# Optimization experiments

Measured on AMD Instinct MI355X. Metric: run time of the kernel, lower is better.

The kernel has to match this reference:

```python
import jax, jax.numpy as jnp
import numpy as np

EPS_NORM = 1e-12  # F.normalize eps
LN_EPS = 1e-5


def _ln(x, g, b):
    mu = x.mean(-1, keepdims=True)
    var = ((x - mu) ** 2).mean(-1, keepdims=True)
    return (x - mu) / jnp.sqrt(var + LN_EPS) * g + b


def _gate(x, w1, b1, g, b, w2, b2):
    # Linear -> LayerNorm(32) -> SiLU -> Linear -> Sigmoid, squeeze(-1)
    t = _ln(x @ w1 + b1, g, b)
    t = jax.nn.silu(t)
    return jax.nn.sigmoid(t @ w2 + b2)[..., 0]


def setup_inputs() -> dict:
    key = jax.random.key(0)
    B, N, D, dH, S, HID = 4, 4096, 1024, 256, 256, 32
    ks = jax.random.split(key, 24)
    sc_d = 0.5 * (6.0 / (D + dH)) ** 0.5  # xavier gain=0.5 approx
    sc_h = 0.5 * (6.0 / (D + HID)) ** 0.5
    inp = {
        "h": jax.random.normal(ks[0], (B, N, D), jnp.float32),
        # encoder complex projection (stored as (in,out))
        "Wr": jax.random.uniform(ks[1], (D, dH), jnp.float32, -sc_d, sc_d),
        "br": jnp.zeros((dH,), jnp.float32),
        "Wi": jax.random.uniform(ks[2], (D, dH), jnp.float32, -sc_d, sc_d),
        "bi": jnp.zeros((dH,), jnp.float32),
        # uncertainty net
        "uw1": jax.random.uniform(ks[3], (D, HID), jnp.float32, -sc_h, sc_h),
        "ub1": jnp.zeros((HID,), jnp.float32),
        "ug": jnp.ones((HID,), jnp.float32),
        "ubeta": jnp.zeros((HID,), jnp.float32),
        "uw2": jax.random.uniform(ks[4], (HID, 1), jnp.float32, -0.2, 0.2),
        "ub2": jnp.zeros((1,), jnp.float32),
        # decoherence gamma net
        "gw1": jax.random.uniform(ks[5], (D, HID), jnp.float32, -sc_h, sc_h),
        "gb1": jnp.zeros((HID,), jnp.float32),
        "gg": jnp.ones((HID,), jnp.float32),
        "gbeta": jnp.zeros((HID,), jnp.float32),
        "gw2": jax.random.uniform(ks[6], (HID, 1), jnp.float32, -0.2, 0.2),
        "gb2": jnp.zeros((1,), jnp.float32),
        # memory attention params
        "m_real": jax.random.normal(ks[7], (S, dH), jnp.float32) / dH ** 0.5,
        "m_imag": jax.random.normal(ks[8], (S, dH), jnp.float32) / dH ** 0.5,
        "values": jax.random.normal(ks[9], (S, D), jnp.float32) * 0.02,
        "ow": jax.random.uniform(ks[10], (D, D), jnp.float32, -0.5 * (3.0 / D) ** 0.5, 0.5 * (3.0 / D) ** 0.5),
        "ob": jnp.zeros((D,), jnp.float32),
        # norms
        "n1g": jnp.ones((D,), jnp.float32),
        "n1b": jnp.zeros((D,), jnp.float32),
        "n2g": jnp.ones((D,), jnp.float32),
        "n2b": jnp.zeros((D,), jnp.float32),
        # FFN
        "fw1": jax.random.normal(ks[11], (D, 4 * D), jnp.float32) * (2.0 / (5 * D)) ** 0.5,
        "fb1": jnp.zeros((4 * D,), jnp.float32),
        "fw2": jax.random.normal(ks[12], (4 * D, D), jnp.float32) * (2.0 / (5 * D)) ** 0.5,
        "fb2": jnp.zeros((D,), jnp.float32),
    }
    return inp


def reference(h, Wr, br, Wi, bi,
              uw1, ub1, ug, ubeta, uw2, ub2,
              gw1, gb1, gg, gbeta, gw2, gb2,
              m_real, m_imag, values, ow, ob,
              n1g, n1b, n2g, n2b, fw1, fb1, fw2, fb2):
    dH = m_real.shape[-1]
    # --- QuantumStateEncoder: psi = normalize(complex(Wr h, Wi h)), p in [0,0.95]
    pr = h @ Wr + br                       # (B,N,dH) real part
    pi = h @ Wi + bi                       # (B,N,dH) imag part
    nrm = jnp.maximum(jnp.sqrt(jnp.sum(pr * pr + pi * pi, -1, keepdims=True)), EPS_NORM)
    pr, pi = pr / nrm, pi / nrm
    p_init = _gate(h, uw1, ub1, ug, ubeta, uw2, ub2) * 0.95   # (B,N)
    # --- ContextualDecoherenceLayer: ctx = mean over N (identical per token)
    ctx = h.mean(axis=1)                   # (B,D)
    gamma = _gate(ctx, gw1, gb1, gg, gbeta, gw2, gb2)          # (B,)
    p = p_init * (1.0 - gamma[:, None])    # (B,N)
    # --- ExternalQuantumMemoryAttention
    mnrm = jnp.maximum(jnp.sqrt(jnp.sum(m_real * m_real + m_imag * m_imag, -1, keepdims=True)), EPS_NORM)
    Mr, Mi = m_real / mnrm, m_imag / mnrm  # (S,dH)
    # <psi|m> = sum conj(psi)*m ; |.|^2 is re^2+im^2
    re = jnp.einsum('bnd,sd->bns', pr, Mr) + jnp.einsum('bnd,sd->bns', pi, Mi)
    im = jnp.einsum('bnd,sd->bns', pr, Mi) - jnp.einsum('bnd,sd->bns', pi, Mr)
    overlap = re * re + im * im            # (B,N,S)
    raw = (1.0 - p)[..., None] * overlap + (p / dH)[..., None]
    attn = raw / (raw.sum(-1, keepdims=True) + 1e-8)
    attn_out = jnp.einsum('bns,sd->bnd', attn, values) @ ow + ob
    # --- residual + LN + FFN (dropout = eval identity)
    h1 = _ln(h + attn_out, n1g, n1b)
    ff = jax.nn.gelu(h1 @ fw1 + fb1, approximate=False) @ fw2 + fb2
    return _ln(h1 + ff, n2g, n2b)
```

## Files before the change

### kernel.cpp

```cpp
#include <hip/hip_runtime.h>
#include <math.h>


#define B_ 4
#define N_ 4096
#define D_ 1024
#define DH_ 256
#define S_ 256
#define HID_ 32
#define M_ (B_ * N_)

typedef unsigned short u16;
typedef unsigned int u32;
typedef __attribute__((ext_vector_type(8))) short bfrag;
typedef __attribute__((ext_vector_type(4))) float ffrag;

__device__ __forceinline__ float b2f(u16 u) {
    return __uint_as_float(((unsigned)u) << 16);
}
__device__ __forceinline__ u16 f2b(float f) {
    unsigned u = __float_as_uint(f);
    return (u16)((u + 0x7FFFu + ((u >> 16) & 1u)) >> 16);
}
__device__ __forceinline__ float fast_erf(float x) {
    float ax = fabsf(x);
    float t = __builtin_amdgcn_rcpf(fmaf(0.3275911f, ax, 1.f));
    float p = t * fmaf(t, fmaf(t, fmaf(t, fmaf(t, 1.061405429f, -1.453152027f),
                                       1.421413741f), -0.284496736f),
                       0.254829592f);
    float e = __expf(-ax * ax);
    float y = fmaf(-p, e, 1.f);
    return copysignf(y, x);
}
__device__ __forceinline__ float gelu_fast(float x) {
    return 0.5f * x * (1.0f + fast_erf(x * 0.70710678118654752440f));
}
__device__ __forceinline__ float ldf(const void* p, size_t i, bool bf) {
    return bf ? b2f(((const u16*)p)[i]) : ((const float*)p)[i];
}
__device__ __forceinline__ bool detect_bf(const void* n1g) {
    return *(const unsigned*)n1g == 0x3F803F80u;
}
__device__ __forceinline__ void gload16(const void* g, void* lds) {
    __builtin_amdgcn_global_load_lds(
        (const __attribute__((address_space(1))) u32*)g,
        (__attribute__((address_space(3))) u32*)lds, 16, 0, 0);
}

__global__ void zero_kernel(float* __restrict__ p, int n) {
    int i = blockIdx.x * 256 + threadIdx.x;
    if (i < n) p[i] = 0.f;
}

__global__ __launch_bounds__(256)
void h2b_kernel(const void* __restrict__ h, u16* __restrict__ hB,
                const void* __restrict__ n1g) {
    const bool bf = detect_bf(n1g);
    const size_t i = ((size_t)blockIdx.x * 256 + threadIdx.x) * 8;
    if (bf) {
        *(uint4*)(hB + i) = *(const uint4*)((const u16*)h + i);
    } else {
        const float* hf = (const float*)h;
        float4 x = *(const float4*)(hf + i);
        float4 y = *(const float4*)(hf + i + 4);
        union { u16 u[8]; uint4 v; } pk;
        pk.u[0] = f2b(x.x); pk.u[1] = f2b(x.y);
        pk.u[2] = f2b(x.z); pk.u[3] = f2b(x.w);
        pk.u[4] = f2b(y.x); pk.u[5] = f2b(y.y);
        pk.u[6] = f2b(y.z); pk.u[7] = f2b(y.w);
        *(uint4*)(hB + i) = pk.v;
    }
}

__global__ void pack_bias_kernel(const void* __restrict__ br,
                                 const void* __restrict__ bi,
                                 void* __restrict__ brbi,
                                 const void* __restrict__ n1g) {
    const bool bf = detect_bf(n1g);
    const int t = threadIdx.x;
    if (bf) {
        ((u16*)brbi)[t]       = ((const u16*)br)[t];
        ((u16*)brbi)[256 + t] = ((const u16*)bi)[t];
    } else {
        ((float*)brbi)[t]       = ((const float*)br)[t];
        ((float*)brbi)[256 + t] = ((const float*)bi)[t];
    }
}

__global__ __launch_bounds__(256)
void transpose_w_kernel(const void* __restrict__ W, u16* __restrict__ WT,
                        int K, int N, const void* __restrict__ n1g) {
    const bool bf = detect_bf(n1g);
    __shared__ u16 t[64][65];
    const int n0 = blockIdx.x * 64, k0 = blockIdx.y * 64;
    const int a = threadIdx.x & 63, b = threadIdx.x >> 6;
#pragma unroll
    for (int r = 0; r < 16; ++r) {
        int k = b * 16 + r;
        t[k][a] = f2b(ldf(W, (size_t)(k0 + k) * N + n0 + a, bf));
    }
    __syncthreads();
#pragma unroll
    for (int r = 0; r < 16; ++r) {
        int n = b * 16 + r;
        WT[(size_t)(n0 + n) * K + k0 + a] = t[a][n];
    }
}

__global__ __launch_bounds__(256)
void ctx_sum_kernel(const u16* __restrict__ hB, float* __restrict__ ctx) {
    const int chunks = N_ / 128;
    const int b = blockIdx.x / chunks;
    const int ch = blockIdx.x % chunks;
    const int tid = threadIdx.x;
    const size_t base = ((size_t)b * N_ + (size_t)ch * 128) * D_;
    float a[4] = {0.f, 0.f, 0.f, 0.f};
    for (int r = 0; r < 128; ++r)
#pragma unroll
        for (int q = 0; q < 4; ++q)
            a[q] += b2f(hB[base + (size_t)r * D_ + q * 256 + tid]);
#pragma unroll
    for (int q = 0; q < 4; ++q)
        atomicAdd(&ctx[b * D_ + q * 256 + tid], a[q]);
}

__global__ __launch_bounds__(128)
void gamma_gate_kernel(const float* __restrict__ ctx,
                       const void* __restrict__ w1, const void* __restrict__ b1,
                       const void* __restrict__ g, const void* __restrict__ beta,
                       const void* __restrict__ w2, const void* __restrict__ b2,
                       float* __restrict__ out, const void* __restrict__ n1g) {
    const bool bf = detect_bf(n1g);
    const int row = blockIdx.x;
    const int tid = threadIdx.x;
    const int col = tid & 31;
    const int chunk = tid >> 5;
    const float xscale = 1.f / (float)N_;

    float acc = 0.f;
    for (int k = chunk * 256; k < chunk * 256 + 256; ++k)
        acc += ctx[(size_t)row * D_ + k] * xscale * ldf(w1, (size_t)k * HID_ + col, bf);

    __shared__ float part[4][HID_];
    __shared__ float s[HID_];
    __shared__ float mu_s, rstd_s;
    part[chunk][col] = acc;
    __syncthreads();
    if (tid < HID_)
        s[tid] = part[0][tid] + part[1][tid] + part[2][tid] + part[3][tid]
               + ldf(b1, tid, bf);
    __syncthreads();
    if (tid == 0) {
        float m = 0.f;
        for (int i = 0; i < HID_; ++i) m += s[i];
        m /= (float)HID_;
        float var = 0.f;
        for (int i = 0; i < HID_; ++i) { float dd = s[i] - m; var += dd * dd; }
        var /= (float)HID_;
        mu_s = m;
        rstd_s = rsqrtf(var + 1e-5f);
    }
    __syncthreads();
    if (tid < HID_) {
        float v = (s[tid] - mu_s) * rstd_s * ldf(g, tid, bf) + ldf(beta, tid, bf);
        v = v / (1.f + expf(-v));
        s[tid] = v * ldf(w2, tid, bf);
    }
    __syncthreads();
    if (tid == 0) {
        float z = 0.f;
        for (int i = 0; i < HID_; ++i) z += s[i];
        z += ldf(b2, 0, bf);
        out[row] = 1.f / (1.f + expf(-z));
    }
}

__global__ __launch_bounds__(128)
void p_gate_kernel(const u16* __restrict__ hB,
                   const void* __restrict__ w1, const void* __restrict__ b1,
                   const void* __restrict__ g, const void* __restrict__ beta,
                   const void* __restrict__ w2, const void* __restrict__ b2,
                   float* __restrict__ out, const void* __restrict__ n1g) {
    const bool bf = detect_bf(n1g);
    const int row = blockIdx.x;
    const int tid = threadIdx.x;
    const int col = tid & 31;
    const int chunk = tid >> 5;

    float acc = 0.f;
    for (int k = chunk * 256; k < chunk * 256 + 256; ++k)
        acc += b2f(hB[(size_t)row * D_ + k]) * ldf(w1, (size_t)k * HID_ + col, bf);

    __shared__ float part[4][HID_];
    __shared__ float s[HID_];
    __shared__ float mu_s, rstd_s;
    part[chunk][col] = acc;
    __syncthreads();
    if (tid < HID_)
        s[tid] = part[0][tid] + part[1][tid] + part[2][tid] + part[3][tid]
               + ldf(b1, tid, bf);
    __syncthreads();
    if (tid == 0) {
        float m = 0.f;
        for (int i = 0; i < HID_; ++i) m += s[i];
        m /= (float)HID_;
        float var = 0.f;
        for (int i = 0; i < HID_; ++i) { float dd = s[i] - m; var += dd * dd; }
        var /= (float)HID_;
        mu_s = m;
        rstd_s = rsqrtf(var + 1e-5f);
    }
    __syncthreads();
    if (tid < HID_) {
        float v = (s[tid] - mu_s) * rstd_s * ldf(g, tid, bf) + ldf(beta, tid, bf);
        v = v / (1.f + expf(-v));
        s[tid] = v * ldf(w2, tid, bf);
    }
    __syncthreads();
    if (tid == 0) {
        float z = 0.f;
        for (int i = 0; i < HID_; ++i) z += s[i];
        z += ldf(b2, 0, bf);
        out[row] = 0.95f / (1.f + expf(-z));
    }
}

__global__ __launch_bounds__(256)
void norm_m_kernel(const void* __restrict__ m_real, const void* __restrict__ m_imag,
                   u16* __restrict__ bcatT, const void* __restrict__ n1g) {
    const bool bf = detect_bf(n1g);
    const int s = blockIdx.x;
    const int d = threadIdx.x;
    float mr = ldf(m_real, (size_t)s * DH_ + d, bf);
    float mi = ldf(m_imag, (size_t)s * DH_ + d, bf);
    float v = mr * mr + mi * mi;
#pragma unroll
    for (int off = 32; off; off >>= 1) v += __shfl_down(v, off, 64);
    __shared__ float red[4];
    if ((d & 63) == 0) red[d >> 6] = v;
    __syncthreads();
    float tot = red[0] + red[1] + red[2] + red[3];
    float inv = 1.f / fmaxf(sqrtf(tot), 1e-12f);
    float nr = mr * inv, ni = mi * inv;
    bcatT[(size_t)s * 512 + d]               = f2b(nr);
    bcatT[(size_t)s * 512 + 256 + d]         = f2b(ni);
    bcatT[(size_t)(256 + s) * 512 + d]       = f2b(ni);
    bcatT[(size_t)(256 + s) * 512 + 256 + d] = f2b(-nr);
}

__global__ __launch_bounds__(256)
void gemm_mfma(const u16* __restrict__ A, const u16* __restrict__ WT,
               const void* __restrict__ bias, void* __restrict__ out,
               int kseg, int lda, int ldw, int ldo,
               int act, int fo32, const void* __restrict__ n1g) {
    const bool bf = detect_bf(n1g);
    __shared__ short As[128 * 64];
    __shared__ short Bs[128 * 64];
    const int tid = threadIdx.x;

    const int nwg = gridDim.x * gridDim.y;
    const int flat = blockIdx.y * gridDim.x + blockIdx.x;
    const int xcd = flat & 7, idx = flat >> 3;
    const int qq = nwg >> 3, rr = nwg & 7;
    const int nf = (xcd < rr ? xcd * (qq + 1) : rr * (qq + 1) + (xcd - rr) * qq) + idx;
    const int c0 = (nf % gridDim.x) * 128;
    const int r0 = (nf / gridDim.x) * 128;

    const int lane = tid & 63, wave = tid >> 6;
    const int wm = wave & 1, wn = wave >> 1;
    const int quad = lane >> 4, l15 = lane & 15;
    const int l8 = lane >> 3;
    const int lc = (lane & 7) ^ l8;
    const int sx = l15 & 7;

    ffrag acc[4][4];
#pragma unroll
    for (int i = 0; i < 4; ++i)
#pragma unroll
        for (int j = 0; j < 4; ++j)
            acc[i][j] = (ffrag){0.f, 0.f, 0.f, 0.f};

    for (int k0 = 0; k0 < kseg; k0 += 64) {
        __syncthreads();
#pragma unroll
        for (int i = 0; i < 4; ++i) {
            int rb = wave * 32 + i * 8;
            gload16(A + (size_t)(r0 + rb + l8) * lda + k0 + lc * 8, &As[rb * 64]);
        }
#pragma unroll
        for (int i = 0; i < 4; ++i) {
            int rb = wave * 32 + i * 8;
            gload16(WT + (size_t)(c0 + rb + l8) * ldw + k0 + lc * 8, &Bs[rb * 64]);
        }
        __syncthreads();

#pragma unroll
        for (int ks = 0; ks < 2; ++ks) {
            bfrag a[4], b[4];
#pragma unroll
            for (int i = 0; i < 4; ++i) {
                int row = wm * 64 + i * 16 + l15;
                a[i] = *(const bfrag*)&As[row * 64 + (((ks * 4 + quad) ^ sx) * 8)];
            }
#pragma unroll
            for (int j = 0; j < 4; ++j) {
                int row = wn * 64 + j * 16 + l15;
                b[j] = *(const bfrag*)&Bs[row * 64 + (((ks * 4 + quad) ^ sx) * 8)];
            }
#pragma unroll
            for (int i = 0; i < 4; ++i)
#pragma unroll
                for (int j = 0; j < 4; ++j)
                    acc[i][j] = __builtin_amdgcn_mfma_f32_16x16x32_bf16(
                        a[i], b[j], acc[i][j], 0, 0, 0);
        }
    }

    float bv[4];
#pragma unroll
    for (int j = 0; j < 4; ++j)
        bv[j] = bias ? ldf(bias, c0 + wn * 64 + j * 16 + l15, bf) : 0.f;
#pragma unroll
    for (int i = 0; i < 4; ++i)
#pragma unroll
        for (int r = 0; r < 4; ++r) {
            int row_g = r0 + wm * 64 + i * 16 + quad * 4 + r;
#pragma unroll
            for (int j = 0; j < 4; ++j) {
                int col_g = c0 + wn * 64 + j * 16 + l15;
                float v = acc[i][j][r] + bv[j];
                if (act) v = gelu_fast(v);
                if (fo32) ((float*)out)[(size_t)row_g * ldo + col_g] = v;
                else      ((u16*)out)[(size_t)row_g * ldo + col_g] = f2b(v);
            }
        }
}

__global__ __launch_bounds__(512, 2)
void gemm_mfma2(const u16* __restrict__ A, const u16* __restrict__ WT,
                const void* __restrict__ bias, void* __restrict__ out,
                int K, int lda, int ldw, int ldo,
                int act, int fo32, const void* __restrict__ n1g) {
    const bool bf = detect_bf(n1g);
    __shared__ short As[2][256 * 64];
    __shared__ short Bs[2][256 * 64];
    const int tid = threadIdx.x;

    const int nwg = gridDim.x * gridDim.y;
    const int flat = blockIdx.y * gridDim.x + blockIdx.x;
    const int xcd = flat & 7, idx = flat >> 3;
    const int qq = nwg >> 3, rr = nwg & 7;
    const int nf = (xcd < rr ? xcd * (qq + 1) : rr * (qq + 1) + (xcd - rr) * qq) + idx;
    const int c0 = (nf % gridDim.x) * 256;
    const int r0 = (nf / gridDim.x) * 256;

    const int lane = tid & 63, wave = tid >> 6;
    const int wm = wave & 1, wn = wave >> 1;
    const int quad = lane >> 4, l15 = lane & 15;
    const int l8 = lane >> 3;
    const int lc = (lane & 7) ^ l8;
    const int sx = l15 & 7;

    ffrag acc[8][4];
#pragma unroll
    for (int i = 0; i < 8; ++i)
#pragma unroll
        for (int j = 0; j < 4; ++j)
            acc[i][j] = (ffrag){0.f, 0.f, 0.f, 0.f};

    auto STAGE = [&](int buf, int k0) {
#pragma unroll
        for (int r = 0; r < 4; ++r) {
            int rb = r * 64 + wave * 8;
            gload16(A + (size_t)(r0 + rb + l8) * lda + k0 + lc * 8,
                    &As[buf][rb * 64]);
        }
#pragma unroll
        for (int r = 0; r < 4; ++r) {
            int rb = r * 64 + wave * 8;
            gload16(WT + (size_t)(c0 + rb + l8) * ldw + k0 + lc * 8,
                    &Bs[buf][rb * 64]);
        }
    };

    const int nt = K >> 6;
    STAGE(0, 0);
    int cur = 0;
    for (int t = 0; t < nt; ++t) {
        if (t + 1 < nt) {
            STAGE(cur ^ 1, (t + 1) << 6);
            asm volatile("s_waitcnt vmcnt(8)" ::: "memory");
        } else {
            asm volatile("s_waitcnt vmcnt(0)" ::: "memory");
        }
        __builtin_amdgcn_s_barrier();
        __builtin_amdgcn_sched_barrier(0);
        __builtin_amdgcn_s_setprio(1);
#pragma unroll
        for (int ks = 0; ks < 2; ++ks) {
            bfrag a[8], b[4];
#pragma unroll
            for (int j = 0; j < 4; ++j) {
                int row = wn * 64 + j * 16 + l15;
                b[j] = *(const bfrag*)&Bs[cur][row * 64 + (((ks * 4 + quad) ^ sx) * 8)];
            }
#pragma unroll
            for (int i = 0; i < 8; ++i) {
                int row = wm * 128 + i * 16 + l15;
                a[i] = *(const bfrag*)&As[cur][row * 64 + (((ks * 4 + quad) ^ sx) * 8)];
#pragma unroll
                for (int j = 0; j < 4; ++j)
                    acc[i][j] = __builtin_amdgcn_mfma_f32_16x16x32_bf16(
                        a[i], b[j], acc[i][j], 0, 0, 0);
            }
        }
        __builtin_amdgcn_s_setprio(0);
        __builtin_amdgcn_sched_barrier(0);
        __builtin_amdgcn_s_barrier();
        cur ^= 1;
    }

    float bv[4];
#pragma unroll
    for (int j = 0; j < 4; ++j)
        bv[j] = bias ? ldf(bias, c0 + wn * 64 + j * 16 + l15, bf) : 0.f;
#pragma unroll
    for (int i = 0; i < 8; ++i)
#pragma unroll
        for (int r = 0; r < 4; ++r) {
            int row_g = r0 + wm * 128 + i * 16 + quad * 4 + r;
#pragma unroll
            for (int j = 0; j < 4; ++j) {
                int col_g = c0 + wn * 64 + j * 16 + l15;
                float v = acc[i][j][r] + bv[j];
                if (act) v = gelu_fast(v);
                if (fo32) ((float*)out)[(size_t)row_g * ldo + col_g] = v;
                else      ((u16*)out)[(size_t)row_g * ldo + col_g] = f2b(v);
            }
        }
}

#define TPW 8
__global__ __launch_bounds__(256)
void attn_weights_kernel(const u16* __restrict__ psi,
                         const float* __restrict__ reim,
                         const float* __restrict__ p_init,
                         const float* __restrict__ gamma,
                         u16* __restrict__ a2) {
    const int token0 = blockIdx.x * TPW;
    const int tid = threadIdx.x;
    __shared__ float red[4];

    for (int tt = 0; tt < TPW; ++tt) {
        const size_t t = (size_t)(token0 + tt);
        float x0 = b2f(psi[t * 512 + tid]);
        float x1 = b2f(psi[t * 512 + 256 + tid]);
        float v = x0 * x0 + x1 * x1;
#pragma unroll
        for (int off = 32; off; off >>= 1) v += __shfl_down(v, off, 64);
        if ((tid & 63) == 0) red[tid >> 6] = v;
        __syncthreads();
        float inv = 1.f / fmaxf(red[0] + red[1] + red[2] + red[3], 1e-24f);

        float p = p_init[t] * (1.f - gamma[t / N_]);
        float re = reim[t * 512 + tid];
        float im = reim[t * 512 + 256 + tid];
        float raw = (1.f - p) * (re * re + im * im) * inv + p * (1.f / (float)DH_);

        float w = raw;
#pragma unroll
        for (int off = 32; off; off >>= 1) w += __shfl_down(w, off, 64);
        __syncthreads();
        if ((tid & 63) == 0) red[tid >> 6] = w;
        __syncthreads();
        float denom = red[0] + red[1] + red[2] + red[3];
        a2[t * 256 + tid] = f2b(raw / (denom + 1e-8f));
        __syncthreads();
    }
}

__global__ __launch_bounds__(256)
void copy_rows_kernel(const u16* __restrict__ src, u16* __restrict__ dst) {
    const int row = blockIdx.x;
    const int tid = threadIdx.x;
#pragma unroll
    for (int q = 0; q < 4; ++q)
        dst[(size_t)row * D_ + q * 256 + tid] = src[(size_t)row * D_ + q * 256 + tid];
}

__global__ __launch_bounds__(256)
void ln_add_kernel(const void* __restrict__ x, int xmode, size_t xrow0,
                   const void* __restrict__ y, int ymode,
                   const void* __restrict__ g, const void* __restrict__ b,
                   u16* __restrict__ outB, float* __restrict__ outF,
                   const void* __restrict__ n1g) {
    const bool bfin = detect_bf(n1g);
    const bool bfx = (xmode == 1) ? true : bfin;
    const int row = blockIdx.x;
    const int tid = threadIdx.x;
    __shared__ float red[4];

    float v[4];
#pragma unroll
    for (int q = 0; q < 4; ++q) {
        int d = q * 256 + tid;
        float yv = ymode ? ((const float*)y)[(size_t)row * D_ + d]
                         : b2f(((const u16*)y)[(size_t)row * D_ + d]);
        v[q] = ldf(x, (xrow0 + row) * (size_t)D_ + d, bfx) + yv;
    }

    float s = v[0] + v[1] + v[2] + v[3];
#pragma unroll
    for (int off = 32; off; off >>= 1) s += __shfl_down(s, off, 64);
    if ((tid & 63) == 0) red[tid >> 6] = s;
    __syncthreads();
    float mu = (red[0] + red[1] + red[2] + red[3]) * (1.f / (float)D_);
    __syncthreads();

    float q2 = 0.f;
#pragma unroll
    for (int j = 0; j < 4; ++j) { float dd = v[j] - mu; q2 += dd * dd; }
#pragma unroll
    for (int off = 32; off; off >>= 1) q2 += __shfl_down(q2, off, 64);
    if ((tid & 63) == 0) red[tid >> 6] = q2;
    __syncthreads();
    float var = (red[0] + red[1] + red[2] + red[3]) * (1.f / (float)D_);
    float rstd = rsqrtf(var + 1e-5f);

#pragma unroll
    for (int q = 0; q < 4; ++q) {
        int d = q * 256 + tid;
        float o = (v[q] - mu) * rstd * ldf(g, d, bfin) + ldf(b, d, bfin);
        if (outF) outF[(size_t)row * D_ + d] = o;
        else      outB[(size_t)row * D_ + d] = f2b(o);
    }
}

extern "C" void kernel_launch(void* const* d_in, const int* in_sizes, int n_in,
                              void* d_out, int out_size, void* d_ws, size_t ws_size,
                              hipStream_t stream) {
    const void* h      = d_in[0];
    const void* Wr     = d_in[1];
    const void* br     = d_in[2];
    const void* Wi     = d_in[3];
    const void* bi     = d_in[4];
    const void* uw1    = d_in[5];
    const void* ub1    = d_in[6];
    const void* ug     = d_in[7];
    const void* ubeta  = d_in[8];
    const void* uw2    = d_in[9];
    const void* ub2    = d_in[10];
    const void* gw1    = d_in[11];
    const void* gb1    = d_in[12];
    const void* gg     = d_in[13];
    const void* gbeta  = d_in[14];
    const void* gw2    = d_in[15];
    const void* gb2    = d_in[16];
    const void* m_real = d_in[17];
    const void* m_imag = d_in[18];
    const void* values = d_in[19];
    const void* ow     = d_in[20];
    const void* ob     = d_in[21];
    const void* n1g    = d_in[22];
    const void* n1b    = d_in[23];
    const void* n2g    = d_in[24];
    const void* n2b    = d_in[25];
    const void* fw1    = d_in[26];
    const void* fb1    = d_in[27];
    const void* fw2    = d_in[28];
    const void* fb2    = d_in[29];

    char*  ws      = (char*)d_ws;
    float* ctx     = (float*)(ws);
    float* gammap  = (float*)(ws + 16384);
    float* p_init  = (float*)(ws + 16448);
    void*  brbi    = (void*)(ws + 81984);
    u16*   BCatT   = (u16*)(ws + 84032);
    u16*   WrT     = (u16*)(ws + 608320);
    u16*   WiT     = (u16*)(ws + 1132608);
    u16*   valuesT = (u16*)(ws + 1656896);
    u16*   owT     = (u16*)(ws + 2181184);
    u16*   fw1T    = (u16*)(ws + 4278336);
    u16*   fw2T    = (u16*)(ws + 12666944);
    const size_t tbase = 21055552;

    int CH = 16384;
    while (CH > 256 && tbase + (size_t)CH * 12288 > ws_size) CH >>= 1;
    u16*   t_buf = (u16*)(ws + tbase);
    float* pf    = (float*)(t_buf + (size_t)CH * 4096);

    float* outF   = (float*)d_out;
    u16*   Psi    = (u16*)d_out;
    u16*   A2     = Psi + (size_t)M_ * 512;
    u16*   X2     = (u16*)d_out + (size_t)M_ * D_;
    u16*   hB     = X2;
    float* REIMf  = (float*)X2;

    h2b_kernel<<<M_ * D_ / 2048, 256, 0, stream>>>(h, hB, n1g);

    transpose_w_kernel<<<dim3(DH_ / 64, D_ / 64), 256, 0, stream>>>(Wr, WrT, D_, DH_, n1g);
    transpose_w_kernel<<<dim3(DH_ / 64, D_ / 64), 256, 0, stream>>>(Wi, WiT, D_, DH_, n1g);
    transpose_w_kernel<<<dim3(D_ / 64, S_ / 64), 256, 0, stream>>>(values, valuesT, S_, D_, n1g);
    transpose_w_kernel<<<dim3(D_ / 64, D_ / 64), 256, 0, stream>>>(ow, owT, D_, D_, n1g);
    transpose_w_kernel<<<dim3(4 * D_ / 64, D_ / 64), 256, 0, stream>>>(fw1, fw1T, D_, 4 * D_, n1g);
    transpose_w_kernel<<<dim3(D_ / 64, 4 * D_ / 64), 256, 0, stream>>>(fw2, fw2T, 4 * D_, D_, n1g);
    pack_bias_kernel<<<1, 256, 0, stream>>>(br, bi, brbi, n1g);

    zero_kernel<<<16, 256, 0, stream>>>(ctx, B_ * D_);
    ctx_sum_kernel<<<B_ * (N_ / 128), 256, 0, stream>>>(hB, ctx);
    gamma_gate_kernel<<<B_, 128, 0, stream>>>(ctx, gw1, gb1, gg, gbeta,
                                              gw2, gb2, gammap, n1g);

    norm_m_kernel<<<S_, 256, 0, stream>>>(m_real, m_imag, BCatT, n1g);

    gemm_mfma<<<dim3(512 / 128, M_ / 128), 256, 0, stream>>>(
        hB, WrT, brbi, Psi, D_, D_, D_, 512, 0, 0, n1g);

    p_gate_kernel<<<M_, 128, 0, stream>>>(hB, uw1, ub1, ug, ubeta,
                                          uw2, ub2, p_init, n1g);

    gemm_mfma<<<dim3(512 / 128, M_ / 128), 256, 0, stream>>>(
        Psi, BCatT, nullptr, REIMf, 512, 512, 512, 512, 0, 1, n1g);

    attn_weights_kernel<<<M_ / TPW, 256, 0, stream>>>(Psi, REIMf, p_init,
                                                      gammap, A2);

    gemm_mfma2<<<dim3(D_ / 256, M_ / 256), 512, 0, stream>>>(
        A2, valuesT, nullptr, X2, S_, S_, S_, D_, 0, 0, n1g);

    for (int c = 0; c < M_ / CH; ++c) {
        const size_t off = (size_t)c * CH * D_;
        gemm_mfma2<<<dim3(D_ / 256, CH / 256), 512, 0, stream>>>(
            X2 + off, owT, ob, pf, D_, D_, D_, D_, 0, 1, n1g);
        ln_add_kernel<<<CH, 256, 0, stream>>>(h, 0, (size_t)c * CH, pf, 1,
                                              n1g, n1b, X2 + off, nullptr, n1g);
    }

    for (int c = 0; c < M_ / CH; ++c) {
        const size_t off = (size_t)c * CH * D_;
        gemm_mfma2<<<dim3(4 * D_ / 256, CH / 256), 512, 0, stream>>>(
            X2 + off, fw1T, fb1, t_buf, D_, D_, D_, 4 * D_, 1, 0, n1g);
        gemm_mfma2<<<dim3(D_ / 256, CH / 256), 512, 0, stream>>>(
            t_buf, fw2T, fb2, pf, 4 * D_, 4 * D_, 4 * D_, D_, 0, 1, n1g);
        copy_rows_kernel<<<CH, 256, 0, stream>>>(X2 + off, t_buf);
        ln_add_kernel<<<CH, 256, 0, stream>>>(t_buf, 1, 0, pf, 1,
                                              n2g, n2b, nullptr, outF + off, n1g);
    }
}
```

Baseline: 1.013 ms.

## Split GEMM k-step into four LDS-load/MFMA phases with barriers and nontemporal stores

The inner GEMM loop now runs four phases per k-tile. Each phase loads a pair of B fragments (and the A fragments on even phases), waits on lgkmcnt, and issues 16 MFMAs at raised priority, with a workgroup barrier after each phase. This is meant to interleave LDS reads and MFMA issue across waves in a ping-pong style. The epilogue stores become nontemporal to avoid cache pollution. The extra barriers could serialize waves and add sync overhead.

```diff
diff --git a/kernel.cpp b/kernel.cpp
--- a/kernel.cpp
+++ b/kernel.cpp
@@ -394,29 +394,38 @@
             asm volatile("s_waitcnt vmcnt(0)" ::: "memory");
         }
         __builtin_amdgcn_s_barrier();
-        __builtin_amdgcn_sched_barrier(0);
-        __builtin_amdgcn_s_setprio(1);
-#pragma unroll
-        for (int ks = 0; ks < 2; ++ks) {
-            bfrag a[8], b[4];
-#pragma unroll
-            for (int j = 0; j < 4; ++j) {
-                int row = wn * 64 + j * 16 + l15;
-                b[j] = *(const bfrag*)&Bs[cur][row * 64 + (((ks * 4 + quad) ^ sx) * 8)];
+
+        bfrag a[8];
+#pragma unroll
+        for (int p = 0; p < 4; ++p) {
+            const int ks = p >> 1;
+            const int jp = (p & 1) * 2;
+            bfrag b2[2];
+#pragma unroll
+            for (int jj = 0; jj < 2; ++jj) {
+                int row = wn * 64 + (jp + jj) * 16 + l15;
+                b2[jj] = *(const bfrag*)&Bs[cur][row * 64 + (((ks * 4 + quad) ^ sx) * 8)];
             }
-#pragma unroll
-            for (int i = 0; i < 8; ++i) {
-                int row = wm * 128 + i * 16 + l15;
-                a[i] = *(const bfrag*)&As[cur][row * 64 + (((ks * 4 + quad) ^ sx) * 8)];
-#pragma unroll
-                for (int j = 0; j < 4; ++j)
-                    acc[i][j] = __builtin_amdgcn_mfma_f32_16x16x32_bf16(
-                        a[i], b[j], acc[i][j], 0, 0, 0);
+            if ((p & 1) == 0) {
+#pragma unroll
+                for (int i = 0; i < 8; ++i) {
+                    int row = wm * 128 + i * 16 + l15;
+                    a[i] = *(const bfrag*)&As[cur][row * 64 + (((ks * 4 + quad) ^ sx) * 8)];
+                }
             }
-        }
-        __builtin_amdgcn_s_setprio(0);
-        __builtin_amdgcn_sched_barrier(0);
-        __builtin_amdgcn_s_barrier();
+            asm volatile("s_waitcnt lgkmcnt(0)" ::: "memory");
+            __builtin_amdgcn_sched_barrier(0);
+            __builtin_amdgcn_s_setprio(1);
+#pragma unroll
+            for (int i = 0; i < 8; ++i)
+#pragma unroll
+                for (int jj = 0; jj < 2; ++jj)
+                    acc[i][jp + jj] = __builtin_amdgcn_mfma_f32_16x16x32_bf16(
+                        a[i], b2[jj], acc[i][jp + jj], 0, 0, 0);
+            __builtin_amdgcn_s_setprio(0);
+            __builtin_amdgcn_sched_barrier(0);
+            __builtin_amdgcn_s_barrier();
+        }
         cur ^= 1;
     }
 
@@ -434,8 +443,12 @@
                 int col_g = c0 + wn * 64 + j * 16 + l15;
                 float v = acc[i][j][r] + bv[j];
                 if (act) v = gelu_fast(v);
-                if (fo32) ((float*)out)[(size_t)row_g * ldo + col_g] = v;
-                else      ((u16*)out)[(size_t)row_g * ldo + col_g] = f2b(v);
+                if (fo32)
+                    __builtin_nontemporal_store(
+                        v, &((float*)out)[(size_t)row_g * ldo + col_g]);
+                else
+                    __builtin_nontemporal_store(
+                        f2b(v), &((u16*)out)[(size_t)row_g * ldo + col_g]);
             }
         }
 }
```

New measurement: 1.099 ms. +8.5%, slower.

## Split GEMM main loop into four phases interleaving global prefetch with MFMA

Applied to the files above, without the earlier changes.

Restructures the 256x256 bf16 GEMM mainloop into four quadrant phases, each loading its own A/B fragments from LDS, issuing one slice of the next tile's global-to-LDS loads, then running 16 MFMAs. This spreads global prefetch across the compute phases instead of issuing it all up front, and cuts live fragment registers. The cost is extra barriers per K-step and more LDS fragment reloads (A fragments are read twice), and vmcnt accounting is more fragile.

```diff
diff --git a/kernel.cpp b/kernel.cpp
--- a/kernel.cpp
+++ b/kernel.cpp
@@ -368,54 +368,80 @@
         for (int j = 0; j < 4; ++j)
             acc[i][j] = (ffrag){0.f, 0.f, 0.f, 0.f};
 
-    auto STAGE = [&](int buf, int k0) {
-#pragma unroll
-        for (int r = 0; r < 4; ++r) {
-            int rb = r * 64 + wave * 8;
-            gload16(A + (size_t)(r0 + rb + l8) * lda + k0 + lc * 8,
-                    &As[buf][rb * 64]);
-        }
-#pragma unroll
-        for (int r = 0; r < 4; ++r) {
-            int rb = r * 64 + wave * 8;
-            gload16(WT + (size_t)(c0 + rb + l8) * ldw + k0 + lc * 8,
-                    &Bs[buf][rb * 64]);
-        }
+    auto STAGE_PIECE = [&](int buf, int k0, int pc) {
+        int rb = pc * 64 + wave * 8;
+        gload16(A + (size_t)(r0 + rb + l8) * lda + k0 + lc * 8,
+                &As[buf][rb * 64]);
+        gload16(WT + (size_t)(c0 + rb + l8) * ldw + k0 + lc * 8,
+                &Bs[buf][rb * 64]);
     };
 
+    bfrag a[4][2], b[2][2];
+    auto PHASE_DS = [&](int buf, int i0, int j0) {
+#pragma unroll
+        for (int jj = 0; jj < 2; ++jj)
+#pragma unroll
+            for (int ks = 0; ks < 2; ++ks) {
+                int row = wn * 64 + (j0 * 2 + jj) * 16 + l15;
+                b[jj][ks] = *(const bfrag*)
+                    &Bs[buf][row * 64 + (((ks * 4 + quad) ^ sx) * 8)];
+            }
+#pragma unroll
+        for (int r = 0; r < 4; ++r)
+#pragma unroll
+            for (int ks = 0; ks < 2; ++ks) {
+                int row = wm * 128 + (i0 * 4 + r) * 16 + l15;
+                a[r][ks] = *(const bfrag*)
+                    &As[buf][row * 64 + (((ks * 4 + quad) ^ sx) * 8)];
+            }
+    };
+    auto PHASE_MFMA = [&](int i0, int j0) {
+#pragma unroll
+        for (int r = 0; r < 4; ++r)
+#pragma unroll
+            for (int jj = 0; jj < 2; ++jj)
+#pragma unroll
+                for (int ks = 0; ks < 2; ++ks)
+                    acc[i0 * 4 + r][j0 * 2 + jj] =
+                        __builtin_amdgcn_mfma_f32_16x16x32_bf16(
+                            a[r][ks], b[jj][ks],
+                            acc[i0 * 4 + r][j0 * 2 + jj], 0, 0, 0);
+    };
+
     const int nt = K >> 6;
-    STAGE(0, 0);
+#pragma unroll
+    for (int pc = 0; pc < 4; ++pc) STAGE_PIECE(0, 0, pc);
     int cur = 0;
     for (int t = 0; t < nt; ++t) {
-        if (t + 1 < nt) {
-            STAGE(cur ^ 1, (t + 1) << 6);
-            asm volatile("s_waitcnt vmcnt(8)" ::: "memory");
+        const int kn = (t + 1) << 6;
+        const bool pre = (t + 1 < nt);
+        if (pre) {
+            STAGE_PIECE(cur ^ 1, kn, 0);
+            asm volatile("s_waitcnt vmcnt(2)" ::: "memory");
         } else {
             asm volatile("s_waitcnt vmcnt(0)" ::: "memory");
         }
         __builtin_amdgcn_s_barrier();
+        PHASE_DS(cur, 0, 0);
+        asm volatile("s_waitcnt lgkmcnt(0)" ::: "memory");
         __builtin_amdgcn_sched_barrier(0);
         __builtin_amdgcn_s_setprio(1);
-#pragma unroll
-        for (int ks = 0; ks < 2; ++ks) {
-            bfrag a[8], b[4];
-#pragma unroll
-            for (int j = 0; j < 4; ++j) {
-                int row = wn * 64 + j * 16 + l15;
-                b[j] = *(const bfrag*)&Bs[cur][row * 64 + (((ks * 4 + quad) ^ sx) * 8)];
-            }
-#pragma unroll
-            for (int i = 0; i < 8; ++i) {
-                int row = wm * 128 + i * 16 + l15;
-                a[i] = *(const bfrag*)&As[cur][row * 64 + (((ks * 4 + quad) ^ sx) * 8)];
-#pragma unroll
-                for (int j = 0; j < 4; ++j)
-                    acc[i][j] = __builtin_amdgcn_mfma_f32_16x16x32_bf16(
-                        a[i], b[j], acc[i][j], 0, 0, 0);
-            }
-        }
+        PHASE_MFMA(0, 0);
         __builtin_amdgcn_s_setprio(0);
         __builtin_amdgcn_sched_barrier(0);
+#pragma unroll
+        for (int p = 1; p < 4; ++p) {
+            const int i0 = p >> 1, j0 = p & 1;
+            PHASE_DS(cur, i0, j0);
+            if (pre) STAGE_PIECE(cur ^ 1, kn, p);
+            __builtin_amdgcn_s_barrier();
+            asm volatile("s_waitcnt lgkmcnt(0)" ::: "memory");
+            __builtin_amdgcn_sched_barrier(0);
+            __builtin_amdgcn_s_setprio(1);
+            PHASE_MFMA(i0, j0);
+            __builtin_amdgcn_s_setprio(0);
+            __builtin_amdgcn_sched_barrier(0);
+        }
         __builtin_amdgcn_s_barrier();
         cur ^= 1;
     }
```

After: 998.8 us. Within noise of the previous version (-1.4%).

## Fold values@ow into one weight and split GEMM k-loop into staged phases

Applied to the files above, without the earlier changes.

Precomputes the product of the memory values and the output projection as a single S×D bf16 weight, so attention output is one GEMM with K=256 from the attention weights instead of two GEMMs (K=256 then K=1024). This removes a full M×D×D GEMM and the intermediate write and read. The main gemm_mfma2 loop is also restructured to interleave LDS fragment loads, MFMA phases and split global prefetch pieces. Folding the two weights changes bf16 rounding of the intermediate, and the finer-grained barriers add some synchronisation.

```diff
diff --git a/kernel.cpp b/kernel.cpp
--- a/kernel.cpp
+++ b/kernel.cpp
@@ -368,52 +368,68 @@
         for (int j = 0; j < 4; ++j)
             acc[i][j] = (ffrag){0.f, 0.f, 0.f, 0.f};
 
-    auto STAGE = [&](int buf, int k0) {
-#pragma unroll
-        for (int r = 0; r < 4; ++r) {
-            int rb = r * 64 + wave * 8;
-            gload16(A + (size_t)(r0 + rb + l8) * lda + k0 + lc * 8,
-                    &As[buf][rb * 64]);
-        }
-#pragma unroll
-        for (int r = 0; r < 4; ++r) {
-            int rb = r * 64 + wave * 8;
-            gload16(WT + (size_t)(c0 + rb + l8) * ldw + k0 + lc * 8,
-                    &Bs[buf][rb * 64]);
-        }
+    auto STAGE_PIECE = [&](int buf, int k0, int pc) {
+        int rb = pc * 64 + wave * 8;
+        gload16(A + (size_t)(r0 + rb + l8) * lda + k0 + lc * 8,
+                &As[buf][rb * 64]);
+        gload16(WT + (size_t)(c0 + rb + l8) * ldw + k0 + lc * 8,
+                &Bs[buf][rb * 64]);
     };
 
+    bfrag a[8], b[4];
+    auto PHASE_DS = [&](int buf, int ks) {
+#pragma unroll
+        for (int j = 0; j < 4; ++j) {
+            int row = wn * 64 + j * 16 + l15;
+            b[j] = *(const bfrag*)&Bs[buf][row * 64 + (((ks * 4 + quad) ^ sx) * 8)];
+        }
+#pragma unroll
+        for (int i = 0; i < 8; ++i) {
+            int row = wm * 128 + i * 16 + l15;
+            a[i] = *(const bfrag*)&As[buf][row * 64 + (((ks * 4 + quad) ^ sx) * 8)];
+        }
+    };
+    auto PHASE_MFMA = [&]() {
+#pragma unroll
+        for (int i = 0; i < 8; ++i)
+#pragma unroll
+            for (int j = 0; j < 4; ++j)
+                acc[i][j] = __builtin_amdgcn_mfma_f32_16x16x32_bf16(
+                    a[i], b[j], acc[i][j], 0, 0, 0);
+    };
+
     const int nt = K >> 6;
-    STAGE(0, 0);
+#pragma unroll
+    for (int pc = 0; pc < 4; ++pc) STAGE_PIECE(0, 0, pc);
     int cur = 0;
     for (int t = 0; t < nt; ++t) {
-        if (t + 1 < nt) {
-            STAGE(cur ^ 1, (t + 1) << 6);
-            asm volatile("s_waitcnt vmcnt(8)" ::: "memory");
+        const int kn = (t + 1) << 6;
+        const bool pre = (t + 1 < nt);
+        if (pre) {
+            STAGE_PIECE(cur ^ 1, kn, 0);
+            STAGE_PIECE(cur ^ 1, kn, 1);
+            asm volatile("s_waitcnt vmcnt(4)" ::: "memory");
         } else {
             asm volatile("s_waitcnt vmcnt(0)" ::: "memory");
         }
         __builtin_amdgcn_s_barrier();
+        PHASE_DS(cur, 0);
+        asm volatile("s_waitcnt lgkmcnt(0)" ::: "memory");
         __builtin_amdgcn_sched_barrier(0);
         __builtin_amdgcn_s_setprio(1);
-#pragma unroll
-        for (int ks = 0; ks < 2; ++ks) {
-            bfrag a[8], b[4];
-#pragma unroll
-            for (int j = 0; j < 4; ++j) {
-                int row = wn * 64 + j * 16 + l15;
-                b[j] = *(const bfrag*)&Bs[cur][row * 64 + (((ks * 4 + quad) ^ sx) * 8)];
-            }
-#pragma unroll
-            for (int i = 0; i < 8; ++i) {
-                int row = wm * 128 + i * 16 + l15;
-                a[i] = *(const bfrag*)&As[cur][row * 64 + (((ks * 4 + quad) ^ sx) * 8)];
-#pragma unroll
-                for (int j = 0; j < 4; ++j)
-                    acc[i][j] = __builtin_amdgcn_mfma_f32_16x16x32_bf16(
-                        a[i], b[j], acc[i][j], 0, 0, 0);
-            }
-        }
+        PHASE_MFMA();
+        __builtin_amdgcn_s_setprio(0);
+        __builtin_amdgcn_sched_barrier(0);
+        PHASE_DS(cur, 1);
+        if (pre) {
+            STAGE_PIECE(cur ^ 1, kn, 2);
+            STAGE_PIECE(cur ^ 1, kn, 3);
+        }
+        __builtin_amdgcn_s_barrier();
+        asm volatile("s_waitcnt lgkmcnt(0)" ::: "memory");
+        __builtin_amdgcn_sched_barrier(0);
+        __builtin_amdgcn_s_setprio(1);
+        PHASE_MFMA();
         __builtin_amdgcn_s_setprio(0);
         __builtin_amdgcn_sched_barrier(0);
         __builtin_amdgcn_s_barrier();
@@ -578,7 +594,6 @@
     u16*   BCatT   = (u16*)(ws + 84032);
     u16*   WrT     = (u16*)(ws + 608320);
     u16*   WiT     = (u16*)(ws + 1132608);
-    u16*   valuesT = (u16*)(ws + 1656896);
     u16*   owT     = (u16*)(ws + 2181184);
     u16*   fw1T    = (u16*)(ws + 4278336);
     u16*   fw2T    = (u16*)(ws + 12666944);
@@ -589,23 +604,28 @@
     u16*   t_buf = (u16*)(ws + tbase);
     float* pf    = (float*)(t_buf + (size_t)CH * 4096);
 
-    float* outF   = (float*)d_out;
-    u16*   Psi    = (u16*)d_out;
-    u16*   A2     = Psi + (size_t)M_ * 512;
-    u16*   X2     = (u16*)d_out + (size_t)M_ * D_;
-    u16*   hB     = X2;
-    float* REIMf  = (float*)X2;
+    float* outF    = (float*)d_out;
+    u16*   Psi     = (u16*)d_out;
+    u16*   A2      = Psi + (size_t)M_ * 512;
+    u16*   VOT     = A2 + (size_t)M_ * 256;
+    u16*   valuesB = VOT + (size_t)D_ * S_;
+    u16*   X2      = (u16*)d_out + (size_t)M_ * D_;
+    u16*   hB      = X2;
+    float* REIMf   = (float*)X2;
 
     h2b_kernel<<<M_ * D_ / 2048, 256, 0, stream>>>(h, hB, n1g);
+    h2b_kernel<<<S_ * D_ / 2048, 256, 0, stream>>>(values, valuesB, n1g);
 
     transpose_w_kernel<<<dim3(DH_ / 64, D_ / 64), 256, 0, stream>>>(Wr, WrT, D_, DH_, n1g);
     transpose_w_kernel<<<dim3(DH_ / 64, D_ / 64), 256, 0, stream>>>(Wi, WiT, D_, DH_, n1g);
-    transpose_w_kernel<<<dim3(D_ / 64, S_ / 64), 256, 0, stream>>>(values, valuesT, S_, D_, n1g);
     transpose_w_kernel<<<dim3(D_ / 64, D_ / 64), 256, 0, stream>>>(ow, owT, D_, D_, n1g);
     transpose_w_kernel<<<dim3(4 * D_ / 64, D_ / 64), 256, 0, stream>>>(fw1, fw1T, D_, 4 * D_, n1g);
     transpose_w_kernel<<<dim3(D_ / 64, 4 * D_ / 64), 256, 0, stream>>>(fw2, fw2T, 4 * D_, D_, n1g);
     pack_bias_kernel<<<1, 256, 0, stream>>>(br, bi, brbi, n1g);
 
+    gemm_mfma<<<dim3(S_ / 128, D_ / 128), 256, 0, stream>>>(
+        owT, valuesB, nullptr, VOT, D_, D_, D_, S_, 0, 0, n1g);
+
     zero_kernel<<<16, 256, 0, stream>>>(ctx, B_ * D_);
     ctx_sum_kernel<<<B_ * (N_ / 128), 256, 0, stream>>>(hB, ctx);
     gamma_gate_kernel<<<B_, 128, 0, stream>>>(ctx, gw1, gb1, gg, gbeta,
@@ -625,15 +645,12 @@
     attn_weights_kernel<<<M_ / TPW, 256, 0, stream>>>(Psi, REIMf, p_init,
                                                       gammap, A2);
 
-    gemm_mfma2<<<dim3(D_ / 256, M_ / 256), 512, 0, stream>>>(
-        A2, valuesT, nullptr, X2, S_, S_, S_, D_, 0, 0, n1g);
-
     for (int c = 0; c < M_ / CH; ++c) {
-        const size_t off = (size_t)c * CH * D_;
+        const size_t offh = (size_t)c * CH * D_;
         gemm_mfma2<<<dim3(D_ / 256, CH / 256), 512, 0, stream>>>(
-            X2 + off, owT, ob, pf, D_, D_, D_, D_, 0, 1, n1g);
+            A2 + (size_t)c * CH * S_, VOT, ob, pf, S_, S_, S_, D_, 0, 1, n1g);
         ln_add_kernel<<<CH, 256, 0, stream>>>(h, 0, (size_t)c * CH, pf, 1,
-                                              n1g, n1b, X2 + off, nullptr, n1g);
+                                              n1g, n1b, X2 + offh, nullptr, n1g);
     }
 
     for (int c = 0; c < M_ / CH; ++c) {
```

Result: faster. 961.6 us (-5.1%).
